# Optimization experiments

Measured on AMD Instinct MI355X. Metric: run time of the kernel, lower is better.

Reference implementation:

```python
import jax, jax.numpy as jnp
import numpy as np

HEADS = 48
HEAD_DIM = 64
DIM = 3072
RANK = 128
TEXT_LEN = 226
VID_LEN = 1822
B = 1
LORA_W = 1.0
EPS = 1e-5


def setup_inputs() -> dict:
    key = jax.random.key(0)
    ks = jax.random.split(key, 24)
    s = 0.02  # weight init scale
    inp = {
        "hidden_states": jax.random.normal(ks[0], (B, VID_LEN, DIM), jnp.float32),
        "encoder_hidden_states": jax.random.normal(ks[1], (B, TEXT_LEN, DIM), jnp.float32),
        "rope_cos": jax.random.uniform(ks[2], (VID_LEN, HEAD_DIM), jnp.float32),
        "rope_sin": jax.random.uniform(ks[3], (VID_LEN, HEAD_DIM), jnp.float32),
        "Wq": jax.random.normal(ks[4], (DIM, DIM), jnp.float32) * s,
        "bq": jax.random.normal(ks[5], (DIM,), jnp.float32) * s,
        "Wk": jax.random.normal(ks[6], (DIM, DIM), jnp.float32) * s,
        "bk": jax.random.normal(ks[7], (DIM,), jnp.float32) * s,
        "Wv": jax.random.normal(ks[8], (DIM, DIM), jnp.float32) * s,
        "bv": jax.random.normal(ks[9], (DIM,), jnp.float32) * s,
        "Wo": jax.random.normal(ks[10], (DIM, DIM), jnp.float32) * s,
        "bo": jax.random.normal(ks[11], (DIM,), jnp.float32) * s,
        "lq_down": jax.random.normal(ks[12], (RANK, DIM), jnp.float32) / RANK,
        "lq_up": jax.random.normal(ks[13], (DIM, RANK), jnp.float32) * s,
        "lk_down": jax.random.normal(ks[14], (RANK, DIM), jnp.float32) / RANK,
        "lk_up": jax.random.normal(ks[15], (DIM, RANK), jnp.float32) * s,
        "lv_down": jax.random.normal(ks[16], (RANK, DIM), jnp.float32) / RANK,
        "lv_up": jax.random.normal(ks[17], (DIM, RANK), jnp.float32) * s,
        "lp_down": jax.random.normal(ks[18], (RANK, DIM), jnp.float32) / RANK,
        "lp_up": jax.random.normal(ks[19], (DIM, RANK), jnp.float32) * s,
        "gamma_q": jnp.ones((HEAD_DIM,), jnp.float32),
        "beta_q": jnp.zeros((HEAD_DIM,), jnp.float32),
        "gamma_k": jnp.ones((HEAD_DIM,), jnp.float32),
        "beta_k": jnp.zeros((HEAD_DIM,), jnp.float32),
    }
    return inp


def _lora(x, down, up):
    # x: [B,S,DIM]; down: [RANK,DIM]; up: [DIM,RANK]
    return (x @ down.T) @ up.T


def _layernorm(x, gamma, beta):
    mu = jnp.mean(x, axis=-1, keepdims=True)
    var = jnp.mean(jnp.square(x - mu), axis=-1, keepdims=True)
    return (x - mu) * jax.lax.rsqrt(var + EPS) * gamma + beta


def _apply_rope(x, cos, sin):
    # diffusers apply_rotary_emb, use_real=True, unbind_dim=-1
    # x: [B,H,S,D]; cos/sin: [S,D]
    xr = x.reshape(*x.shape[:-1], HEAD_DIM // 2, 2)
    x1, x2 = xr[..., 0], xr[..., 1]
    x_rot = jnp.stack([-x2, x1], axis=-1).reshape(x.shape)
    return x * cos + x_rot * sin


def reference(hidden_states, encoder_hidden_states, rope_cos, rope_sin,
              Wq, bq, Wk, bk, Wv, bv, Wo, bo,
              lq_down, lq_up, lk_down, lk_up, lv_down, lv_up, lp_down, lp_up,
              gamma_q, beta_q, gamma_k, beta_k):
    h = jnp.concatenate([encoder_hidden_states, hidden_states], axis=1)  # [B,S,DIM]
    S = h.shape[1]

    q = h @ Wq.T + bq + _lora(h, lq_down, lq_up) * LORA_W
    k = h @ Wk.T + bk + _lora(h, lk_down, lk_up) * LORA_W
    v = h @ Wv.T + bv + _lora(h, lv_down, lv_up) * LORA_W

    def split_heads(x):  # [B,S,DIM] -> [B,H,S,D]
        return x.reshape(B, S, HEADS, HEAD_DIM).transpose(0, 2, 1, 3)

    q, k, v = split_heads(q), split_heads(k), split_heads(v)
    q = _layernorm(q, gamma_q, beta_q)
    k = _layernorm(k, gamma_k, beta_k)

    # RoPE on video tokens only
    q = q.at[:, :, TEXT_LEN:].set(_apply_rope(q[:, :, TEXT_LEN:], rope_cos, rope_sin))
    k = k.at[:, :, TEXT_LEN:].set(_apply_rope(k[:, :, TEXT_LEN:], rope_cos, rope_sin))

    # scaled dot-product attention (no mask, no dropout)
    scale = 1.0 / np.sqrt(HEAD_DIM).astype(np.float32)
    scores = jnp.einsum("bhqd,bhkd->bhqk", q, k) * scale
    probs = jax.nn.softmax(scores, axis=-1)
    attn_out = jnp.einsum("bhqk,bhkd->bhqd", probs, v)

    out = attn_out.transpose(0, 2, 1, 3).reshape(B, S, DIM)
    out = out @ Wo.T + bo + _lora(out, lp_down, lp_up) * LORA_W

    enc_out = out[:, :TEXT_LEN, :]
    hid_out = out[:, TEXT_LEN:, :]
    return (hid_out, enc_out)
```

## Files before the change

### kernel.cpp

```cpp
#include <hip/hip_runtime.h>
#include <hip/hip_bf16.h>
#include <stdint.h>

#define S_TOT 2048
#define TEXT 226
#define VID 1822
#define DIM 3072
#define NH 48
#define HD 64

typedef __bf16 bf16x8 __attribute__((ext_vector_type(8)));
typedef float f32x4 __attribute__((ext_vector_type(4)));

#define AS1 __attribute__((address_space(1)))
#define AS3 __attribute__((address_space(3)))

__device__ __forceinline__ void g2l16(const void* g, void* l) {
    __builtin_amdgcn_global_load_lds((const AS1 uint32_t*)(uintptr_t)g,
                                     (AS3 uint32_t*)(uintptr_t)l, 16, 0, 0);
}

#define ARENA_N 47431680ull

struct NormArgs { const void* p[24]; };

__global__ __launch_bounds__(256)
void normalize_inputs(NormArgs a, __bf16* __restrict__ arena)
{
    static constexpr unsigned long long segStart[25] = {
        0ull, 694272ull, 6291456ull, 15728640ull, 25165824ull, 34603008ull,
        44040192ull, 44433408ull, 44826624ull, 45219840ull, 45613056ull,
        46006272ull, 46399488ull, 46792704ull, 47185920ull, 47302528ull,
        47419136ull, 47422208ull, 47425280ull, 47428352ull, 47431424ull,
        47431488ull, 47431552ull, 47431616ull, 47431680ull };
    static constexpr int segIn[24] = {
        1, 0, 4, 6, 8, 10, 12, 13, 14, 15, 16, 17, 18, 19, 2, 3,
        5, 7, 9, 11, 20, 21, 22, 23 };

    const uint32_t w0 = *(const uint32_t*)a.p[20];
    const bool f32in = (w0 == 0x3F800000u);

    const size_t i0 = ((size_t)blockIdx.x * 256 + threadIdx.x) * 8;
    if (i0 >= ARENA_N) return;
    int s = 0;
    while (i0 >= segStart[s + 1]) s++;
    const size_t off = i0 - segStart[s];

    if (f32in) {
        const float* src = (const float*)a.p[segIn[s]] + off;
        const float4 v0 = ((const float4*)src)[0];
        const float4 v1 = ((const float4*)src)[1];
        bf16x8 o;
        o[0] = (__bf16)v0.x; o[1] = (__bf16)v0.y; o[2] = (__bf16)v0.z; o[3] = (__bf16)v0.w;
        o[4] = (__bf16)v1.x; o[5] = (__bf16)v1.y; o[6] = (__bf16)v1.z; o[7] = (__bf16)v1.w;
        *(bf16x8*)(arena + i0) = o;
    } else {
        const __bf16* src = (const __bf16*)a.p[segIn[s]] + off;
        *(uint4*)(arena + i0) = *(const uint4*)src;
    }
}

template<bool ADD, bool ATOMIC>
__global__ __launch_bounds__(256)
void gemm_bt(const __bf16* __restrict__ A, int lda, int aGroupStride,
             const __bf16* __restrict__ B0, const __bf16* __restrict__ B1,
             const __bf16* __restrict__ B2, int ldb,
             const __bf16* __restrict__ bias0, const __bf16* __restrict__ bias1,
             const __bf16* __restrict__ bias2,
             float* __restrict__ C, int ldc,
             int K, int tilesPerGroup, int kChunk)
{
    __shared__ __bf16 As[128 * 32];
    __shared__ __bf16 Bs[128 * 32];
    const int tid  = threadIdx.x;
    const int wave = tid >> 6;
    const int lane = tid & 63;
    const int l15  = lane & 15, quad = lane >> 4;
    const int bm = blockIdx.x, bn = blockIdx.y;
    const int group = bn / tilesPerGroup;
    const int nt    = bn - group * tilesPerGroup;
    const __bf16* B    = (group == 0) ? B0 : ((group == 1) ? B1 : B2);
    const __bf16* bias = (group == 0) ? bias0 : ((group == 1) ? bias1 : bias2);
    const __bf16* Ae   = A + (size_t)group * aGroupStride;

    const int k0s = blockIdx.z * kChunk;
    int k0e = k0s + kChunk; if (k0e > K) k0e = K;

    const int srow = lane >> 2;
    const int schk = (lane & 3) * 8;
    const __bf16* Ag = Ae + (size_t)(bm * 128) * lda + schk;
    const __bf16* Bg = B  + (size_t)(nt * 128) * ldb + schk;

    f32x4 acc[4][4] = {};
    const int wm = (wave & 1) * 64;
    const int wn = (wave >> 1) * 64;

    for (int k0 = k0s; k0 < k0e; k0 += 32) {
        __syncthreads();
#pragma unroll
        for (int i = 0; i < 2; i++) {
            const int blk = i * 4 + wave;
            const int r = blk * 16 + srow;
            g2l16(Ag + (size_t)r * lda + k0, &As[blk * 512]);
            g2l16(Bg + (size_t)r * ldb + k0, &Bs[blk * 512]);
        }
        __syncthreads();
        bf16x8 af[4], bfr[4];
#pragma unroll
        for (int i = 0; i < 4; i++)
            af[i] = *(const bf16x8*)&As[(wm + i * 16 + l15) * 32 + quad * 8];
#pragma unroll
        for (int j = 0; j < 4; j++)
            bfr[j] = *(const bf16x8*)&Bs[(wn + j * 16 + l15) * 32 + quad * 8];
#pragma unroll
        for (int i = 0; i < 4; i++)
#pragma unroll
            for (int j = 0; j < 4; j++)
                acc[i][j] = __builtin_amdgcn_mfma_f32_16x16x32_bf16(af[i], bfr[j], acc[i][j], 0, 0, 0);
    }

#pragma unroll
    for (int i = 0; i < 4; i++) {
#pragma unroll
        for (int j = 0; j < 4; j++) {
            const int coll = wn + j * 16 + l15;
            const int col  = bn * 128 + coll;
            float bv = 0.f;
            if (bias) bv = (float)bias[nt * 128 + coll];
#pragma unroll
            for (int r = 0; r < 4; r++) {
                const int row = bm * 128 + wm + i * 16 + quad * 4 + r;
                float v = acc[i][j][r] + bv;
                float* p = C + (size_t)row * ldc + col;
                if (ATOMIC)      atomicAdd(p, v);
                else if (ADD)    *p += v;
                else             *p = v;
            }
        }
    }
}

__global__ __launch_bounds__(256)
void ln_rope(const float* __restrict__ qkv,
             const __bf16* __restrict__ gq, const __bf16* __restrict__ bq,
             const __bf16* __restrict__ gk, const __bf16* __restrict__ bk,
             const __bf16* __restrict__ cosb, const __bf16* __restrict__ sinb,
             __bf16* __restrict__ qh, __bf16* __restrict__ kh)
{
    const int s = blockIdx.x;
    const int wave = threadIdx.x >> 6, lane = threadIdx.x & 63;
    for (int idx = wave; idx < 2 * NH; idx += 4) {
        const int mat  = idx / NH;
        const int head = idx - mat * NH;
        float x = qkv[(size_t)s * 9216 + mat * DIM + head * HD + lane];
        float mu = x;
        mu += __shfl_xor(mu, 1, 64);  mu += __shfl_xor(mu, 2, 64);
        mu += __shfl_xor(mu, 4, 64);  mu += __shfl_xor(mu, 8, 64);
        mu += __shfl_xor(mu, 16, 64); mu += __shfl_xor(mu, 32, 64);
        mu *= 0.015625f;
        float d = x - mu;
        float vv = d * d;
        vv += __shfl_xor(vv, 1, 64);  vv += __shfl_xor(vv, 2, 64);
        vv += __shfl_xor(vv, 4, 64);  vv += __shfl_xor(vv, 8, 64);
        vv += __shfl_xor(vv, 16, 64); vv += __shfl_xor(vv, 32, 64);
        vv *= 0.015625f;
        const float g = (float)(mat ? gk[lane] : gq[lane]);
        const float b = (float)(mat ? bk[lane] : bq[lane]);
        float y = d * rsqrtf(vv + 1e-5f) * g + b;
        if (s >= TEXT) {
            const int pos = s - TEXT;
            const float c  = (float)cosb[pos * HD + lane];
            const float sn = (float)sinb[pos * HD + lane];
            const float oth = __shfl_xor(y, 1, 64);
            const float rot = (lane & 1) ? oth : -oth;
            y = y * c + rot * sn;
        }
        __bf16* dst = mat ? kh : qh;
        dst[((size_t)head * S_TOT + s) * HD + lane] = (__bf16)y;
    }
}

__global__ __launch_bounds__(256)
void vtrans(const float* __restrict__ qkv, __bf16* __restrict__ vt)
{
    __shared__ float tile[64][65];
    const int h = blockIdx.x, sb = blockIdx.y;
    const int tid = threadIdx.x;
    const int r0 = tid >> 4;
    const int c0 = (tid & 15) * 4;
#pragma unroll
    for (int p = 0; p < 4; p++) {
        const int r = p * 16 + r0;
        const float4 v = *(const float4*)&qkv[((size_t)(sb * 64 + r)) * 9216 + 2 * DIM + h * HD + c0];
        tile[r][c0 + 0] = v.x; tile[r][c0 + 1] = v.y;
        tile[r][c0 + 2] = v.z; tile[r][c0 + 3] = v.w;
    }
    __syncthreads();
#pragma unroll
    for (int p = 0; p < 4; p++) {
        const int d = p * 16 + r0;
        __bf16 o[4];
#pragma unroll
        for (int e = 0; e < 4; e++) o[e] = (__bf16)tile[c0 + e][d];
        *(uint2*)&vt[((size_t)(h * HD + d)) * S_TOT + sb * 64 + c0] = *(const uint2*)o;
    }
}

#define KS_LD 72
#define VS_LD 136
#define PS_LD 136

__global__ __launch_bounds__(256)
void flash_attn(const __bf16* __restrict__ qh, const __bf16* __restrict__ kh,
                const __bf16* __restrict__ vt, __bf16* __restrict__ outp)
{
    __shared__ __bf16 Ks[128 * KS_LD];
    __shared__ __bf16 Vs[64 * VS_LD];
    __shared__ __bf16 Ps[4 * 32 * PS_LD];
    const int qb = blockIdx.x, h = blockIdx.y;
    const int tid = threadIdx.x, wave = tid >> 6, lane = tid & 63;
    const int l15 = lane & 15, quad = lane >> 4;

    bf16x8 qf[2][2];
#pragma unroll
    for (int t = 0; t < 2; t++)
#pragma unroll
        for (int ks = 0; ks < 2; ks++) {
            const __bf16* p = qh + ((size_t)(h * S_TOT + qb * 128 + wave * 32 + t * 16 + l15)) * HD
                                 + ks * 32 + quad * 8;
            bf16x8 v = *(const bf16x8*)p;
#pragma unroll
            for (int e = 0; e < 8; e++) v[e] = (__bf16)((float)v[e] * 0.125f);
            qf[t][ks] = v;
        }

    f32x4 of[2][4] = {};
    float m_i[2][4], l_i[2][4];
#pragma unroll
    for (int t = 0; t < 2; t++)
#pragma unroll
        for (int r = 0; r < 4; r++) { m_i[t][r] = -1e30f; l_i[t][r] = 0.f; }

    for (int kb = 0; kb < S_TOT / 128; kb++) {
        bf16x8 kr[4], vr[4];
#pragma unroll
        for (int p = 0; p < 4; p++) {
            const int id = p * 256 + tid;
            const int krow = id >> 3, kc = (id & 7) * 8;
            kr[p] = *(const bf16x8*)(kh + ((size_t)(h * S_TOT + kb * 128 + krow)) * HD + kc);
            const int vrow = id >> 4, vc = (id & 15) * 8;
            vr[p] = *(const bf16x8*)(vt + ((size_t)(h * HD + vrow)) * S_TOT + kb * 128 + vc);
        }
        __syncthreads();
#pragma unroll
        for (int p = 0; p < 4; p++) {
            const int id = p * 256 + tid;
            const int krow = id >> 3, kc = (id & 7) * 8;
            *(bf16x8*)&Ks[krow * KS_LD + kc] = kr[p];
            const int vrow = id >> 4, vc = (id & 15) * 8;
            *(bf16x8*)&Vs[vrow * VS_LD + vc] = vr[p];
        }
        __syncthreads();

        f32x4 sf[2][8];
#pragma unroll
        for (int n = 0; n < 8; n++) {
            const bf16x8 k0 = *(const bf16x8*)&Ks[(n * 16 + l15) * KS_LD + quad * 8];
            const bf16x8 k1 = *(const bf16x8*)&Ks[(n * 16 + l15) * KS_LD + 32 + quad * 8];
            f32x4 z0 = {0.f, 0.f, 0.f, 0.f};
            f32x4 z1 = {0.f, 0.f, 0.f, 0.f};
            z0 = __builtin_amdgcn_mfma_f32_16x16x32_bf16(qf[0][0], k0, z0, 0, 0, 0);
            sf[0][n] = __builtin_amdgcn_mfma_f32_16x16x32_bf16(qf[0][1], k1, z0, 0, 0, 0);
            z1 = __builtin_amdgcn_mfma_f32_16x16x32_bf16(qf[1][0], k0, z1, 0, 0, 0);
            sf[1][n] = __builtin_amdgcn_mfma_f32_16x16x32_bf16(qf[1][1], k1, z1, 0, 0, 0);
        }

        const float L2E = 1.44269504f;
#pragma unroll
        for (int t = 0; t < 2; t++) {
#pragma unroll
            for (int r = 0; r < 4; r++) {
                float mx = sf[t][0][r];
#pragma unroll
                for (int n = 1; n < 8; n++) mx = fmaxf(mx, sf[t][n][r]);
                mx = fmaxf(mx, __shfl_xor(mx, 1, 64));
                mx = fmaxf(mx, __shfl_xor(mx, 2, 64));
                mx = fmaxf(mx, __shfl_xor(mx, 4, 64));
                mx = fmaxf(mx, __shfl_xor(mx, 8, 64));
                const float mnew = fmaxf(m_i[t][r], mx);
                const float alpha = __builtin_amdgcn_exp2f((m_i[t][r] - mnew) * L2E);
                m_i[t][r] = mnew;
                float rs = 0.f;
#pragma unroll
                for (int n = 0; n < 8; n++) {
                    const float pv = __builtin_amdgcn_exp2f((sf[t][n][r] - mnew) * L2E);
                    sf[t][n][r] = pv;
                    rs += pv;
                }
                rs += __shfl_xor(rs, 1, 64);
                rs += __shfl_xor(rs, 2, 64);
                rs += __shfl_xor(rs, 4, 64);
                rs += __shfl_xor(rs, 8, 64);
                l_i[t][r] = l_i[t][r] * alpha + rs;
#pragma unroll
                for (int j = 0; j < 4; j++) of[t][j][r] *= alpha;
            }
        }

        __bf16* Pw = Ps + wave * (32 * PS_LD);
#pragma unroll
        for (int t = 0; t < 2; t++)
#pragma unroll
            for (int n = 0; n < 8; n++)
#pragma unroll
                for (int r = 0; r < 4; r++)
                    Pw[(t * 16 + quad * 4 + r) * PS_LD + n * 16 + l15] = (__bf16)sf[t][n][r];

#pragma unroll
        for (int kk = 0; kk < 4; kk++) {
            const bf16x8 pf0 = *(const bf16x8*)&Pw[(l15) * PS_LD + kk * 32 + quad * 8];
            const bf16x8 pf1 = *(const bf16x8*)&Pw[(16 + l15) * PS_LD + kk * 32 + quad * 8];
#pragma unroll
            for (int j = 0; j < 4; j++) {
                const bf16x8 vf = *(const bf16x8*)&Vs[(j * 16 + l15) * VS_LD + kk * 32 + quad * 8];
                of[0][j] = __builtin_amdgcn_mfma_f32_16x16x32_bf16(pf0, vf, of[0][j], 0, 0, 0);
                of[1][j] = __builtin_amdgcn_mfma_f32_16x16x32_bf16(pf1, vf, of[1][j], 0, 0, 0);
            }
        }
    }

#pragma unroll
    for (int t = 0; t < 2; t++)
#pragma unroll
        for (int r = 0; r < 4; r++) {
            const float inv = 1.f / l_i[t][r];
            const int row = qb * 128 + wave * 32 + t * 16 + quad * 4 + r;
#pragma unroll
            for (int j = 0; j < 4; j++)
                outp[(size_t)row * DIM + h * HD + j * 16 + l15] = (__bf16)(of[t][j][r] * inv);
        }
}

__global__ __launch_bounds__(256)
void f32_to_bf16(const float* __restrict__ src, __bf16* __restrict__ dst, int n4)
{
    const int i = blockIdx.x * blockDim.x + threadIdx.x;
    if (i < n4) {
        const float4 v = ((const float4*)src)[i];
        __bf16 o[4] = {(__bf16)v.x, (__bf16)v.y, (__bf16)v.z, (__bf16)v.w};
        ((uint2*)dst)[i] = *(const uint2*)o;
    }
}

__global__ __launch_bounds__(256)
void reorder_out(const float* __restrict__ out2, void* __restrict__ doutv,
                 const void* __restrict__ dtype_probe)
{
    const bool f32out = (*(const uint32_t*)dtype_probe == 0x3F800000u);
    const int s = blockIdx.x;
    const size_t dst = (s < TEXT) ? ((size_t)VID * DIM + (size_t)s * DIM)
                                  : ((size_t)(s - TEXT) * DIM);
    const float* src = out2 + (size_t)s * DIM;
#pragma unroll
    for (int p = 0; p < 3; p++) {
        const int c = (p * 256 + threadIdx.x) * 4;
        const float4 v = *(const float4*)&src[c];
        if (f32out) {
            *(float4*)&((float*)doutv)[dst + c] = v;
        } else {
            __bf16 o[4] = {(__bf16)v.x, (__bf16)v.y, (__bf16)v.z, (__bf16)v.w};
            *(uint2*)&((__bf16*)doutv)[dst + c] = *(const uint2*)o;
        }
    }
}

extern "C" void kernel_launch(void* const* d_in, const int* in_sizes, int n_in,
                              void* d_out, int out_size, void* d_ws, size_t ws_size,
                              hipStream_t stream)
{
    char* ws = (char*)d_ws;
    __bf16* arena = (__bf16*)ws;

    const __bf16* h     = arena + 0;
    const __bf16* Wq    = arena + 6291456;
    const __bf16* Wk    = arena + 15728640;
    const __bf16* Wv    = arena + 25165824;
    const __bf16* Wo    = arena + 34603008;
    const __bf16* lqd   = arena + 44040192;
    const __bf16* lqu   = arena + 44433408;
    const __bf16* lkd   = arena + 44826624;
    const __bf16* lku   = arena + 45219840;
    const __bf16* lvd   = arena + 45613056;
    const __bf16* lvu   = arena + 46006272;
    const __bf16* lpd   = arena + 46399488;
    const __bf16* lpu   = arena + 46792704;
    const __bf16* ropec = arena + 47185920;
    const __bf16* ropes = arena + 47302528;
    const __bf16* bq    = arena + 47419136;
    const __bf16* bk    = arena + 47422208;
    const __bf16* bv    = arena + 47425280;
    const __bf16* bo    = arena + 47428352;
    const __bf16* gq    = arena + 47431424;
    const __bf16* btq   = arena + 47431488;
    const __bf16* gk    = arena + 47431552;
    const __bf16* btk   = arena + 47431616;

    float*  qkvf = (float*)(ws + 94863360);
    float*  out2 = (float*)(ws + 94863360);
    float*  t32  = (float*)(ws + 170360832);
    __bf16* t16  = (__bf16*)(ws + 174555136);
    __bf16* qh   = (__bf16*)(ws + 176652288);
    __bf16* kh   = (__bf16*)(ws + 189235200);
    __bf16* vt   = (__bf16*)(ws + 201818112);
    __bf16* attn = (__bf16*)(ws + 0);

    NormArgs na;
    for (int i = 0; i < 24; i++) na.p[i] = d_in[i];
    normalize_inputs<<<(unsigned)((ARENA_N / 8 + 255) / 256), 256, 0, stream>>>(na, arena);

    hipMemsetAsync(t32, 0, (size_t)2048 * 512 * 4, stream);

    gemm_bt<false, false><<<dim3(16, 72, 1), 256, 0, stream>>>(
        h, DIM, 0, Wq, Wk, Wv, DIM, bq, bk, bv, qkvf, 9216, DIM, 24, DIM);
    gemm_bt<false, true><<<dim3(16, 3, 4), 256, 0, stream>>>(
        h, DIM, 0, lqd, lkd, lvd, DIM, nullptr, nullptr, nullptr, t32, 512, DIM, 1, 768);
    f32_to_bf16<<<(2048 * 512 / 4 + 255) / 256, 256, 0, stream>>>(t32, t16, 2048 * 512 / 4);
    gemm_bt<true, false><<<dim3(16, 72, 1), 256, 0, stream>>>(
        t16, 512, 128, lqu, lku, lvu, 128, nullptr, nullptr, nullptr, qkvf, 9216, 128, 24, 128);

    ln_rope<<<2048, 256, 0, stream>>>(qkvf, gq, btq, gk, btk, ropec, ropes, qh, kh);
    vtrans<<<dim3(48, 32), 256, 0, stream>>>(qkvf, vt);
    flash_attn<<<dim3(16, 48), 256, 0, stream>>>(qh, kh, vt, attn);

    gemm_bt<false, false><<<dim3(16, 24, 1), 256, 0, stream>>>(
        attn, DIM, 0, Wo, Wo, Wo, DIM, bo, bo, bo, out2, DIM, DIM, 24, DIM);
    gemm_bt<false, true><<<dim3(16, 1, 4), 256, 0, stream>>>(
        attn, DIM, 0, lpd, lpd, lpd, DIM, nullptr, nullptr, nullptr, t32 + 384, 512, DIM, 1, 768);
    f32_to_bf16<<<(2048 * 512 / 4 + 255) / 256, 256, 0, stream>>>(t32, t16, 2048 * 512 / 4);
    gemm_bt<true, false><<<dim3(16, 24, 1), 256, 0, stream>>>(
        t16 + 384, 512, 0, lpu, lpu, lpu, 128, nullptr, nullptr, nullptr, out2, DIM, 128, 24, 128);

    reorder_out<<<2048, 256, 0, stream>>>(out2, d_out, d_in[20]);
}
```

Baseline: 828.2 us.

## Fuse LoRA-up into main GEMMs, write output directly, keep P in registers

The LoRA up-projection is folded into the main QKV and output GEMMs as a second K-loop over the same accumulators. This removes the separate read-modify-write pass over the fp32 result and the standalone reorder/convert kernel, since the output GEMM now writes straight into the final layout. Flash attention computes S transposed (K as the A operand) so each lane holds one query row's scores. P can then feed a 16x16x16 MFMA directly from registers without the LDS round-trip, and the softmax reductions need only two cross-lane shuffles. In exchange the PV product uses the narrower MFMA instruction, and per-row alpha and l values must be broadcast with shuffles.

```diff
diff --git a/kernel.cpp b/kernel.cpp
--- a/kernel.cpp
+++ b/kernel.cpp
@@ -10,6 +10,7 @@
 #define HD 64
 
 typedef __bf16 bf16x8 __attribute__((ext_vector_type(8)));
+typedef __bf16 bf16x4 __attribute__((ext_vector_type(4)));
 typedef float f32x4 __attribute__((ext_vector_type(4)));
 
 #define AS1 __attribute__((address_space(1)))
@@ -18,6 +19,20 @@
 __device__ __forceinline__ void g2l16(const void* g, void* l) {
     __builtin_amdgcn_global_load_lds((const AS1 uint32_t*)(uintptr_t)g,
                                      (AS3 uint32_t*)(uintptr_t)l, 16, 0, 0);
+}
+
+__device__ __forceinline__ f32x4 mfma16(bf16x4 a, bf16x4 b, f32x4 c) {
+#if __has_builtin(__builtin_amdgcn_mfma_f32_16x16x16bf16_1k)
+    typedef short s4 __attribute__((ext_vector_type(4)));
+    union U { bf16x4 b; s4 s; };
+    U ua, ub; ua.b = a; ub.b = b;
+    return __builtin_amdgcn_mfma_f32_16x16x16bf16_1k(ua.s, ub.s, c, 0, 0, 0);
+#else
+    f32x4 d = c;
+    asm volatile("v_mfma_f32_16x16x16_bf16 %0, %1, %2, %0"
+                 : "+v"(d) : "v"(a), "v"(b));
+    return d;
+#endif
 }
 
 #define ARENA_N 47431680ull
@@ -60,15 +75,49 @@
     }
 }
 
-template<bool ADD, bool ATOMIC>
-__global__ __launch_bounds__(256)
-void gemm_bt(const __bf16* __restrict__ A, int lda, int aGroupStride,
+__device__ __forceinline__ void mm_chunks(
+    const __bf16* __restrict__ Ag, int lda, const __bf16* __restrict__ Bg, int ldb,
+    int kbeg, int kend, f32x4 (&acc)[4][4], __bf16* As, __bf16* Bs,
+    int wave, int srow, int l15, int quad, int wm, int wn)
+{
+    for (int k0 = kbeg; k0 < kend; k0 += 32) {
+        __syncthreads();
+#pragma unroll
+        for (int i = 0; i < 2; i++) {
+            const int blk = i * 4 + wave;
+            const int r = blk * 16 + srow;
+            g2l16(Ag + (size_t)r * lda + k0, &As[blk * 512]);
+            g2l16(Bg + (size_t)r * ldb + k0, &Bs[blk * 512]);
+        }
+        __syncthreads();
+        bf16x8 af[4], bfr[4];
+#pragma unroll
+        for (int i = 0; i < 4; i++)
+            af[i] = *(const bf16x8*)&As[(wm + i * 16 + l15) * 32 + quad * 8];
+#pragma unroll
+        for (int j = 0; j < 4; j++)
+            bfr[j] = *(const bf16x8*)&Bs[(wn + j * 16 + l15) * 32 + quad * 8];
+#pragma unroll
+        for (int i = 0; i < 4; i++)
+#pragma unroll
+            for (int j = 0; j < 4; j++)
+                acc[i][j] = __builtin_amdgcn_mfma_f32_16x16x32_bf16(af[i], bfr[j], acc[i][j], 0, 0, 0);
+    }
+}
+
+template<bool ATOMIC, bool FUSE2, bool TO_OUT>
+__global__ __launch_bounds__(256)
+void gemm_bt(const __bf16* __restrict__ A, int lda,
              const __bf16* __restrict__ B0, const __bf16* __restrict__ B1,
              const __bf16* __restrict__ B2, int ldb,
              const __bf16* __restrict__ bias0, const __bf16* __restrict__ bias1,
              const __bf16* __restrict__ bias2,
+             const __bf16* __restrict__ A2, int lda2, int a2ColOff,
+             const __bf16* __restrict__ U0, const __bf16* __restrict__ U1,
+             const __bf16* __restrict__ U2, int ldu,
              float* __restrict__ C, int ldc,
-             int K, int tilesPerGroup, int kChunk)
+             int K, int K2, int tilesPerGroup, int kChunk,
+             void* __restrict__ dout, const void* __restrict__ probe)
 {
     __shared__ __bf16 As[128 * 32];
     __shared__ __bf16 Bs[128 * 32];
@@ -81,43 +130,30 @@
     const int nt    = bn - group * tilesPerGroup;
     const __bf16* B    = (group == 0) ? B0 : ((group == 1) ? B1 : B2);
     const __bf16* bias = (group == 0) ? bias0 : ((group == 1) ? bias1 : bias2);
-    const __bf16* Ae   = A + (size_t)group * aGroupStride;
 
     const int k0s = blockIdx.z * kChunk;
     int k0e = k0s + kChunk; if (k0e > K) k0e = K;
 
     const int srow = lane >> 2;
     const int schk = (lane & 3) * 8;
-    const __bf16* Ag = Ae + (size_t)(bm * 128) * lda + schk;
-    const __bf16* Bg = B  + (size_t)(nt * 128) * ldb + schk;
+    const __bf16* Ag = A + (size_t)(bm * 128) * lda + schk;
+    const __bf16* Bg = B + (size_t)(nt * 128) * ldb + schk;
 
     f32x4 acc[4][4] = {};
     const int wm = (wave & 1) * 64;
     const int wn = (wave >> 1) * 64;
 
-    for (int k0 = k0s; k0 < k0e; k0 += 32) {
-        __syncthreads();
-#pragma unroll
-        for (int i = 0; i < 2; i++) {
-            const int blk = i * 4 + wave;
-            const int r = blk * 16 + srow;
-            g2l16(Ag + (size_t)r * lda + k0, &As[blk * 512]);
-            g2l16(Bg + (size_t)r * ldb + k0, &Bs[blk * 512]);
-        }
-        __syncthreads();
-        bf16x8 af[4], bfr[4];
-#pragma unroll
-        for (int i = 0; i < 4; i++)
-            af[i] = *(const bf16x8*)&As[(wm + i * 16 + l15) * 32 + quad * 8];
-#pragma unroll
-        for (int j = 0; j < 4; j++)
-            bfr[j] = *(const bf16x8*)&Bs[(wn + j * 16 + l15) * 32 + quad * 8];
-#pragma unroll
-        for (int i = 0; i < 4; i++)
-#pragma unroll
-            for (int j = 0; j < 4; j++)
-                acc[i][j] = __builtin_amdgcn_mfma_f32_16x16x32_bf16(af[i], bfr[j], acc[i][j], 0, 0, 0);
-    }
+    mm_chunks(Ag, lda, Bg, ldb, k0s, k0e, acc, As, Bs, wave, srow, l15, quad, wm, wn);
+
+    if (FUSE2) {
+        const __bf16* U = (group == 0) ? U0 : ((group == 1) ? U1 : U2);
+        const __bf16* A2g = A2 + group * a2ColOff + (size_t)(bm * 128) * lda2 + schk;
+        const __bf16* Ug  = U + (size_t)(nt * 128) * ldu + schk;
+        mm_chunks(A2g, lda2, Ug, ldu, 0, K2, acc, As, Bs, wave, srow, l15, quad, wm, wn);
+    }
+
+    bool f32out = false;
+    if (TO_OUT) f32out = (*(const uint32_t*)probe == 0x3F800000u);
 
 #pragma unroll
     for (int i = 0; i < 4; i++) {
@@ -131,10 +167,15 @@
             for (int r = 0; r < 4; r++) {
                 const int row = bm * 128 + wm + i * 16 + quad * 4 + r;
                 float v = acc[i][j][r] + bv;
-                float* p = C + (size_t)row * ldc + col;
-                if (ATOMIC)      atomicAdd(p, v);
-                else if (ADD)    *p += v;
-                else             *p = v;
+                if (TO_OUT) {
+                    const size_t mrow = (row < TEXT) ? (size_t)(row + VID) : (size_t)(row - TEXT);
+                    if (f32out) ((float*)dout)[mrow * DIM + col] = v;
+                    else        ((__bf16*)dout)[mrow * DIM + col] = (__bf16)v;
+                } else if (ATOMIC) {
+                    atomicAdd(C + (size_t)row * ldc + col, v);
+                } else {
+                    C[(size_t)row * ldc + col] = v;
+                }
             }
         }
     }
@@ -208,7 +249,6 @@
 
 #define KS_LD 72
 #define VS_LD 136
-#define PS_LD 136
 
 __global__ __launch_bounds__(256)
 void flash_attn(const __bf16* __restrict__ qh, const __bf16* __restrict__ kh,
@@ -216,7 +256,6 @@
 {
     __shared__ __bf16 Ks[128 * KS_LD];
     __shared__ __bf16 Vs[64 * VS_LD];
-    __shared__ __bf16 Ps[4 * 32 * PS_LD];
     const int qb = blockIdx.x, h = blockIdx.y;
     const int tid = threadIdx.x, wave = tid >> 6, lane = tid & 63;
     const int l15 = lane & 15, quad = lane >> 4;
@@ -235,11 +274,9 @@
         }
 
     f32x4 of[2][4] = {};
-    float m_i[2][4], l_i[2][4];
-#pragma unroll
-    for (int t = 0; t < 2; t++)
-#pragma unroll
-        for (int r = 0; r < 4; r++) { m_i[t][r] = -1e30f; l_i[t][r] = 0.f; }
+    float m_i[2] = {-1e30f, -1e30f};
+    float l_i[2] = {0.f, 0.f};
+    const float L2E = 1.44269504f;
 
     for (int kb = 0; kb < S_TOT / 128; kb++) {
         bf16x8 kr[4], vr[4];
@@ -267,64 +304,68 @@
         for (int n = 0; n < 8; n++) {
             const bf16x8 k0 = *(const bf16x8*)&Ks[(n * 16 + l15) * KS_LD + quad * 8];
             const bf16x8 k1 = *(const bf16x8*)&Ks[(n * 16 + l15) * KS_LD + 32 + quad * 8];
-            f32x4 z0 = {0.f, 0.f, 0.f, 0.f};
-            f32x4 z1 = {0.f, 0.f, 0.f, 0.f};
-            z0 = __builtin_amdgcn_mfma_f32_16x16x32_bf16(qf[0][0], k0, z0, 0, 0, 0);
-            sf[0][n] = __builtin_amdgcn_mfma_f32_16x16x32_bf16(qf[0][1], k1, z0, 0, 0, 0);
-            z1 = __builtin_amdgcn_mfma_f32_16x16x32_bf16(qf[1][0], k0, z1, 0, 0, 0);
-            sf[1][n] = __builtin_amdgcn_mfma_f32_16x16x32_bf16(qf[1][1], k1, z1, 0, 0, 0);
-        }
-
-        const float L2E = 1.44269504f;
+#pragma unroll
+            for (int t = 0; t < 2; t++) {
+                f32x4 z = {0.f, 0.f, 0.f, 0.f};
+                z = __builtin_amdgcn_mfma_f32_16x16x32_bf16(k0, qf[t][0], z, 0, 0, 0);
+                sf[t][n] = __builtin_amdgcn_mfma_f32_16x16x32_bf16(k1, qf[t][1], z, 0, 0, 0);
+            }
+        }
+
+        float alpha_l[2];
 #pragma unroll
         for (int t = 0; t < 2; t++) {
-#pragma unroll
-            for (int r = 0; r < 4; r++) {
-                float mx = sf[t][0][r];
-#pragma unroll
-                for (int n = 1; n < 8; n++) mx = fmaxf(mx, sf[t][n][r]);
-                mx = fmaxf(mx, __shfl_xor(mx, 1, 64));
-                mx = fmaxf(mx, __shfl_xor(mx, 2, 64));
-                mx = fmaxf(mx, __shfl_xor(mx, 4, 64));
-                mx = fmaxf(mx, __shfl_xor(mx, 8, 64));
-                const float mnew = fmaxf(m_i[t][r], mx);
-                const float alpha = __builtin_amdgcn_exp2f((m_i[t][r] - mnew) * L2E);
-                m_i[t][r] = mnew;
-                float rs = 0.f;
-#pragma unroll
-                for (int n = 0; n < 8; n++) {
+            float mx = sf[t][0][0];
+#pragma unroll
+            for (int n = 0; n < 8; n++)
+#pragma unroll
+                for (int r = 0; r < 4; r++) mx = fmaxf(mx, sf[t][n][r]);
+            mx = fmaxf(mx, __shfl_xor(mx, 16, 64));
+            mx = fmaxf(mx, __shfl_xor(mx, 32, 64));
+            const float mnew = fmaxf(m_i[t], mx);
+            alpha_l[t] = __builtin_amdgcn_exp2f((m_i[t] - mnew) * L2E);
+            m_i[t] = mnew;
+            float rs = 0.f;
+#pragma unroll
+            for (int n = 0; n < 8; n++)
+#pragma unroll
+                for (int r = 0; r < 4; r++) {
                     const float pv = __builtin_amdgcn_exp2f((sf[t][n][r] - mnew) * L2E);
                     sf[t][n][r] = pv;
                     rs += pv;
                 }
-                rs += __shfl_xor(rs, 1, 64);
-                rs += __shfl_xor(rs, 2, 64);
-                rs += __shfl_xor(rs, 4, 64);
-                rs += __shfl_xor(rs, 8, 64);
-                l_i[t][r] = l_i[t][r] * alpha + rs;
-#pragma unroll
-                for (int j = 0; j < 4; j++) of[t][j][r] *= alpha;
+            rs += __shfl_xor(rs, 16, 64);
+            rs += __shfl_xor(rs, 32, 64);
+            l_i[t] = l_i[t] * alpha_l[t] + rs;
+        }
+
+        bf16x4 pf[2][8];
+#pragma unroll
+        for (int t = 0; t < 2; t++)
+#pragma unroll
+            for (int kk = 0; kk < 8; kk++) {
+                bf16x4 o;
+                o[0] = (__bf16)sf[t][kk][0]; o[1] = (__bf16)sf[t][kk][1];
+                o[2] = (__bf16)sf[t][kk][2]; o[3] = (__bf16)sf[t][kk][3];
+                pf[t][kk] = o;
             }
-        }
-
-        __bf16* Pw = Ps + wave * (32 * PS_LD);
+
 #pragma unroll
         for (int t = 0; t < 2; t++)
 #pragma unroll
-            for (int n = 0; n < 8; n++)
-#pragma unroll
-                for (int r = 0; r < 4; r++)
-                    Pw[(t * 16 + quad * 4 + r) * PS_LD + n * 16 + l15] = (__bf16)sf[t][n][r];
-
-#pragma unroll
-        for (int kk = 0; kk < 4; kk++) {
-            const bf16x8 pf0 = *(const bf16x8*)&Pw[(l15) * PS_LD + kk * 32 + quad * 8];
-            const bf16x8 pf1 = *(const bf16x8*)&Pw[(16 + l15) * PS_LD + kk * 32 + quad * 8];
+            for (int r = 0; r < 4; r++) {
+                const float a_r = __shfl(alpha_l[t], quad * 4 + r, 16);
+#pragma unroll
+                for (int j = 0; j < 4; j++) of[t][j][r] *= a_r;
+            }
+
+#pragma unroll
+        for (int kk = 0; kk < 8; kk++) {
 #pragma unroll
             for (int j = 0; j < 4; j++) {
-                const bf16x8 vf = *(const bf16x8*)&Vs[(j * 16 + l15) * VS_LD + kk * 32 + quad * 8];
-                of[0][j] = __builtin_amdgcn_mfma_f32_16x16x32_bf16(pf0, vf, of[0][j], 0, 0, 0);
-                of[1][j] = __builtin_amdgcn_mfma_f32_16x16x32_bf16(pf1, vf, of[1][j], 0, 0, 0);
+                const bf16x4 vf = *(const bf16x4*)&Vs[(j * 16 + l15) * VS_LD + kk * 16 + quad * 4];
+                of[0][j] = mfma16(pf[0][kk], vf, of[0][j]);
+                of[1][j] = mfma16(pf[1][kk], vf, of[1][j]);
             }
         }
     }
@@ -333,7 +374,8 @@
     for (int t = 0; t < 2; t++)
 #pragma unroll
         for (int r = 0; r < 4; r++) {
-            const float inv = 1.f / l_i[t][r];
+            const float lr = __shfl(l_i[t], quad * 4 + r, 16);
+            const float inv = 1.f / lr;
             const int row = qb * 128 + wave * 32 + t * 16 + quad * 4 + r;
 #pragma unroll
             for (int j = 0; j < 4; j++)
@@ -349,28 +391,6 @@
         const float4 v = ((const float4*)src)[i];
         __bf16 o[4] = {(__bf16)v.x, (__bf16)v.y, (__bf16)v.z, (__bf16)v.w};
         ((uint2*)dst)[i] = *(const uint2*)o;
-    }
-}
-
-__global__ __launch_bounds__(256)
-void reorder_out(const float* __restrict__ out2, void* __restrict__ doutv,
-                 const void* __restrict__ dtype_probe)
-{
-    const bool f32out = (*(const uint32_t*)dtype_probe == 0x3F800000u);
-    const int s = blockIdx.x;
-    const size_t dst = (s < TEXT) ? ((size_t)VID * DIM + (size_t)s * DIM)
-                                  : ((size_t)(s - TEXT) * DIM);
-    const float* src = out2 + (size_t)s * DIM;
-#pragma unroll
-    for (int p = 0; p < 3; p++) {
-        const int c = (p * 256 + threadIdx.x) * 4;
-        const float4 v = *(const float4*)&src[c];
-        if (f32out) {
-            *(float4*)&((float*)doutv)[dst + c] = v;
-        } else {
-            __bf16 o[4] = {(__bf16)v.x, (__bf16)v.y, (__bf16)v.z, (__bf16)v.w};
-            *(uint2*)&((__bf16*)doutv)[dst + c] = *(const uint2*)o;
-        }
     }
 }
 
@@ -406,7 +426,6 @@
     const __bf16* btk   = arena + 47431616;
 
     float*  qkvf = (float*)(ws + 94863360);
-    float*  out2 = (float*)(ws + 94863360);
     float*  t32  = (float*)(ws + 170360832);
     __bf16* t16  = (__bf16*)(ws + 174555136);
     __bf16* qh   = (__bf16*)(ws + 176652288);
@@ -420,25 +439,29 @@
 
     hipMemsetAsync(t32, 0, (size_t)2048 * 512 * 4, stream);
 
-    gemm_bt<false, false><<<dim3(16, 72, 1), 256, 0, stream>>>(
-        h, DIM, 0, Wq, Wk, Wv, DIM, bq, bk, bv, qkvf, 9216, DIM, 24, DIM);
-    gemm_bt<false, true><<<dim3(16, 3, 4), 256, 0, stream>>>(
-        h, DIM, 0, lqd, lkd, lvd, DIM, nullptr, nullptr, nullptr, t32, 512, DIM, 1, 768);
+    gemm_bt<true, false, false><<<dim3(16, 3, 4), 256, 0, stream>>>(
+        h, DIM, lqd, lkd, lvd, DIM, nullptr, nullptr, nullptr,
+        nullptr, 0, 0, nullptr, nullptr, nullptr, 0,
+        t32, 512, DIM, 0, 1, 768, nullptr, nullptr);
     f32_to_bf16<<<(2048 * 512 / 4 + 255) / 256, 256, 0, stream>>>(t32, t16, 2048 * 512 / 4);
-    gemm_bt<true, false><<<dim3(16, 72, 1), 256, 0, stream>>>(
-        t16, 512, 128, lqu, lku, lvu, 128, nullptr, nullptr, nullptr, qkvf, 9216, 128, 24, 128);
+
+    gemm_bt<false, true, false><<<dim3(16, 72, 1), 256, 0, stream>>>(
+        h, DIM, Wq, Wk, Wv, DIM, bq, bk, bv,
+        t16, 512, 128, lqu, lku, lvu, 128,
+        qkvf, 9216, DIM, 128, 24, DIM, nullptr, nullptr);
 
     ln_rope<<<2048, 256, 0, stream>>>(qkvf, gq, btq, gk, btk, ropec, ropes, qh, kh);
     vtrans<<<dim3(48, 32), 256, 0, stream>>>(qkvf, vt);
     flash_attn<<<dim3(16, 48), 256, 0, stream>>>(qh, kh, vt, attn);
 
-    gemm_bt<false, false><<<dim3(16, 24, 1), 256, 0, stream>>>(
-        attn, DIM, 0, Wo, Wo, Wo, DIM, bo, bo, bo, out2, DIM, DIM, 24, DIM);
-    gemm_bt<false, true><<<dim3(16, 1, 4), 256, 0, stream>>>(
-        attn, DIM, 0, lpd, lpd, lpd, DIM, nullptr, nullptr, nullptr, t32 + 384, 512, DIM, 1, 768);
+    gemm_bt<true, false, false><<<dim3(16, 1, 4), 256, 0, stream>>>(
+        attn, DIM, lpd, lpd, lpd, DIM, nullptr, nullptr, nullptr,
+        nullptr, 0, 0, nullptr, nullptr, nullptr, 0,
+        t32 + 384, 512, DIM, 0, 1, 768, nullptr, nullptr);
     f32_to_bf16<<<(2048 * 512 / 4 + 255) / 256, 256, 0, stream>>>(t32, t16, 2048 * 512 / 4);
-    gemm_bt<true, false><<<dim3(16, 24, 1), 256, 0, stream>>>(
-        t16 + 384, 512, 0, lpu, lpu, lpu, 128, nullptr, nullptr, nullptr, out2, DIM, 128, 24, 128);
-
-    reorder_out<<<2048, 256, 0, stream>>>(out2, d_out, d_in[20]);
-}
+
+    gemm_bt<false, true, true><<<dim3(16, 24, 1), 256, 0, stream>>>(
+        attn, DIM, Wo, Wo, Wo, DIM, bo, bo, bo,
+        t16 + 384, 512, 0, lpu, lpu, lpu, 128,
+        nullptr, 0, DIM, 128, 24, DIM, d_out, d_in[20]);
+}
```

After: 716.3 us. 13.5% less time.
